# Kernel optimization log

Hardware: AMD Instinct MI355X
Metric: run time of the kernel (lower is better)

## Reference

```python
import jax, jax.numpy as jnp
import numpy as np

N_CLASSES = 3

def setup_inputs() -> dict:
    key = jax.random.key(0)
    k1, k2 = jax.random.split(key)
    feats = jax.random.normal(k1, (16, 1024, 1024, 3), dtype=jnp.float32)
    inst = jax.random.randint(k2, (16, 1024, 1024, 1), 0, N_CLASSES, dtype=jnp.int32)
    return {"feats": feats, "inst": inst}

def reference(feats, inst):
    # Faithful to the TF layer: for each class c, compute the GLOBAL mean of
    # feats over all masked elements (mask tiled across the 3 channels, over
    # the whole batch), then scatter that scalar back into masked positions.
    # Class masks are disjoint, so the sequential update order is benign.
    for c in range(N_CLASSES):
        mask = (inst == c)                                   # [B,H,W,1]
        maskb = jnp.broadcast_to(mask, feats.shape)          # [B,H,W,3]
        cnt = jnp.sum(maskb.astype(feats.dtype))             # scalar count (incl. channels)
        feats_mean = jnp.sum(jnp.where(maskb, feats, 0)) / cnt
        feats = jnp.where(maskb, feats_mean, feats)
    return feats
```

## Files before the change

### kernel.cpp

```cpp
#include <hip/hip_runtime.h>


#define RBLK 2048

typedef float vfloat4 __attribute__((ext_vector_type(4)));
typedef int vint4 __attribute__((ext_vector_type(4)));

__device__ inline double wred_d(double v) {
#pragma unroll
    for (int off = 32; off; off >>= 1) v += __shfl_down(v, off, 64);
    return v;
}
__device__ inline unsigned wred_u(unsigned v) {
#pragma unroll
    for (int off = 32; off; off >>= 1) v += __shfl_down(v, off, 64);
    return v;
}

__global__ __launch_bounds__(256) void reduce_k(const float* __restrict__ feats,
                                                const int* __restrict__ inst,
                                                double* __restrict__ psum,
                                                unsigned* __restrict__ pcnt,
                                                unsigned char* __restrict__ codes,
                                                int npix4) {
    int tid = blockIdx.x * 256 + threadIdx.x;
    int stride = gridDim.x * 256;
    double s0 = 0.0, s1 = 0.0, s2 = 0.0;
    unsigned c0 = 0, c1 = 0, c2 = 0;
    const vint4* inst4 = (const vint4*)inst;
    for (int i = tid; i < npix4; i += stride) {
        vint4 cls = inst4[i];
        const vfloat4* f = (const vfloat4*)(feats + (size_t)i * 12);
        vfloat4 a = f[0], b = f[1], c = f[2];
        double d0 = (double)(a.x + a.y + a.z);
        double d1 = (double)(a.w + b.x + b.y);
        double d2 = (double)(b.z + b.w + c.x);
        double d3 = (double)(c.y + c.z + c.w);
        s0 += (cls.x == 0) ? d0 : 0.0;
        s1 += (cls.x == 1) ? d0 : 0.0;
        s2 += (cls.x == 2) ? d0 : 0.0;
        s0 += (cls.y == 0) ? d1 : 0.0;
        s1 += (cls.y == 1) ? d1 : 0.0;
        s2 += (cls.y == 2) ? d1 : 0.0;
        s0 += (cls.z == 0) ? d2 : 0.0;
        s1 += (cls.z == 1) ? d2 : 0.0;
        s2 += (cls.z == 2) ? d2 : 0.0;
        s0 += (cls.w == 0) ? d3 : 0.0;
        s1 += (cls.w == 1) ? d3 : 0.0;
        s2 += (cls.w == 2) ? d3 : 0.0;
        c0 += (unsigned)(cls.x == 0) + (unsigned)(cls.y == 0) +
              (unsigned)(cls.z == 0) + (unsigned)(cls.w == 0);
        c1 += (unsigned)(cls.x == 1) + (unsigned)(cls.y == 1) +
              (unsigned)(cls.z == 1) + (unsigned)(cls.w == 1);
        c2 += (unsigned)(cls.x == 2) + (unsigned)(cls.y == 2) +
              (unsigned)(cls.z == 2) + (unsigned)(cls.w == 2);
        codes[i] = (unsigned char)((cls.x & 3) | ((cls.y & 3) << 2) |
                                   ((cls.z & 3) << 4) | ((cls.w & 3) << 6));
    }
    s0 = wred_d(s0); s1 = wred_d(s1); s2 = wred_d(s2);
    c0 = wred_u(c0); c1 = wred_u(c1); c2 = wred_u(c2);

    __shared__ double ls[4][3];
    __shared__ unsigned lc[4][3];
    int wid = threadIdx.x >> 6;
    int lane = threadIdx.x & 63;
    if (lane == 0) {
        ls[wid][0] = s0; ls[wid][1] = s1; ls[wid][2] = s2;
        lc[wid][0] = c0; lc[wid][1] = c1; lc[wid][2] = c2;
    }
    __syncthreads();
    if (threadIdx.x < 3) {
        int c = threadIdx.x;
        double s = ls[0][c] + ls[1][c] + ls[2][c] + ls[3][c];
        unsigned cc = lc[0][c] + lc[1][c] + lc[2][c] + lc[3][c];
        psum[blockIdx.x * 3 + c] = s;
        pcnt[blockIdx.x * 3 + c] = cc;
    }
}

__global__ __launch_bounds__(256) void finalize_k(const double* __restrict__ psum,
                                                  const unsigned* __restrict__ pcnt,
                                                  float* __restrict__ mean,
                                                  int nblk) {
    double s0 = 0.0, s1 = 0.0, s2 = 0.0;
    unsigned c0 = 0, c1 = 0, c2 = 0;
    for (int i = threadIdx.x; i < nblk; i += 256) {
        s0 += psum[i * 3 + 0]; s1 += psum[i * 3 + 1]; s2 += psum[i * 3 + 2];
        c0 += pcnt[i * 3 + 0]; c1 += pcnt[i * 3 + 1]; c2 += pcnt[i * 3 + 2];
    }
    s0 = wred_d(s0); s1 = wred_d(s1); s2 = wred_d(s2);
    c0 = wred_u(c0); c1 = wred_u(c1); c2 = wred_u(c2);

    __shared__ double ls[4][3];
    __shared__ unsigned lc[4][3];
    int wid = threadIdx.x >> 6;
    int lane = threadIdx.x & 63;
    if (lane == 0) {
        ls[wid][0] = s0; ls[wid][1] = s1; ls[wid][2] = s2;
        lc[wid][0] = c0; lc[wid][1] = c1; lc[wid][2] = c2;
    }
    __syncthreads();
    if (threadIdx.x < 3) {
        int c = threadIdx.x;
        double s = ls[0][c] + ls[1][c] + ls[2][c] + ls[3][c];
        unsigned cc = lc[0][c] + lc[1][c] + lc[2][c] + lc[3][c];
        mean[c] = (float)(s / (3.0 * (double)cc));
    }
}

__global__ __launch_bounds__(256) void scatter_k(const unsigned short* __restrict__ codes2,
                                                 const float* __restrict__ mean,
                                                 float* __restrict__ out,
                                                 int npix8) {
    int i = blockIdx.x * 256 + threadIdx.x;
    if (i >= npix8) return;
    float m0 = mean[0], m1 = mean[1], m2 = mean[2];
    unsigned cc = codes2[i];
    float v[8];
#pragma unroll
    for (int p = 0; p < 8; ++p) {
        unsigned k = (cc >> (2 * p)) & 3;
        v[p] = (k == 1) ? m1 : ((k == 2) ? m2 : m0);
    }
    vfloat4* o = (vfloat4*)(out + (size_t)i * 24);
    vfloat4 o0 = {v[0], v[0], v[0], v[1]};
    vfloat4 o1 = {v[1], v[1], v[2], v[2]};
    vfloat4 o2 = {v[2], v[3], v[3], v[3]};
    vfloat4 o3 = {v[4], v[4], v[4], v[5]};
    vfloat4 o4 = {v[5], v[5], v[6], v[6]};
    vfloat4 o5 = {v[6], v[7], v[7], v[7]};
    o[0] = o0; o[1] = o1; o[2] = o2; o[3] = o3; o[4] = o4; o[5] = o5;
}

extern "C" void kernel_launch(void* const* d_in, const int* in_sizes, int n_in,
                              void* d_out, int out_size, void* d_ws, size_t ws_size,
                              hipStream_t stream) {
    const float* feats = (const float*)d_in[0];
    const int* inst = (const int*)d_in[1];
    float* out = (float*)d_out;

    int npix = in_sizes[1];
    int npix4 = npix >> 2;
    int npix8 = npix >> 3;

    double* psum = (double*)d_ws;
    unsigned* pcnt = (unsigned*)(psum + RBLK * 3);
    float* mean = (float*)(pcnt + RBLK * 3);
    unsigned char* codes = (unsigned char*)(mean + 4);

    reduce_k<<<RBLK, 256, 0, stream>>>(feats, inst, psum, pcnt, codes, npix4);
    finalize_k<<<1, 256, 0, stream>>>(psum, pcnt, mean, RBLK);
    scatter_k<<<(npix8 + 255) / 256, 256, 0, stream>>>((const unsigned short*)codes, mean,
                                                       out, npix8);
}
```

Baseline: 415.9 us.

## Fuse finalize into scatter and process 8 pixels per reduce iteration

Removes the single-block finalize kernel: every scatter block now redundantly reduces the 2048 per-block partials to compute the class means in shared memory, then writes the output in a grid-stride loop over a fixed grid. The reduce kernel now handles 8 pixels per iteration and writes 16-bit codes directly. This saves one kernel launch and the serial single-block gap, at the cost of each scatter block re-reading the partial sums (about 72KB per block, mostly served from cache).

```diff
diff --git a/kernel.cpp b/kernel.cpp
--- a/kernel.cpp
+++ b/kernel.cpp
@@ -17,45 +17,58 @@
     return v;
 }
 
+__device__ inline void acc_group(vint4 cls, vfloat4 a, vfloat4 b, vfloat4 c,
+                                 double& s0, double& s1, double& s2,
+                                 unsigned& c0, unsigned& c1, unsigned& c2) {
+    double d0 = (double)(a.x + a.y + a.z);
+    double d1 = (double)(a.w + b.x + b.y);
+    double d2 = (double)(b.z + b.w + c.x);
+    double d3 = (double)(c.y + c.z + c.w);
+    s0 += (cls.x == 0) ? d0 : 0.0;
+    s1 += (cls.x == 1) ? d0 : 0.0;
+    s2 += (cls.x == 2) ? d0 : 0.0;
+    s0 += (cls.y == 0) ? d1 : 0.0;
+    s1 += (cls.y == 1) ? d1 : 0.0;
+    s2 += (cls.y == 2) ? d1 : 0.0;
+    s0 += (cls.z == 0) ? d2 : 0.0;
+    s1 += (cls.z == 1) ? d2 : 0.0;
+    s2 += (cls.z == 2) ? d2 : 0.0;
+    s0 += (cls.w == 0) ? d3 : 0.0;
+    s1 += (cls.w == 1) ? d3 : 0.0;
+    s2 += (cls.w == 2) ? d3 : 0.0;
+    c0 += (unsigned)(cls.x == 0) + (unsigned)(cls.y == 0) +
+          (unsigned)(cls.z == 0) + (unsigned)(cls.w == 0);
+    c1 += (unsigned)(cls.x == 1) + (unsigned)(cls.y == 1) +
+          (unsigned)(cls.z == 1) + (unsigned)(cls.w == 1);
+    c2 += (unsigned)(cls.x == 2) + (unsigned)(cls.y == 2) +
+          (unsigned)(cls.z == 2) + (unsigned)(cls.w == 2);
+}
+
+__device__ inline unsigned pack4(vint4 cls) {
+    return (unsigned)((cls.x & 3) | ((cls.y & 3) << 2) |
+                      ((cls.z & 3) << 4) | ((cls.w & 3) << 6));
+}
+
 __global__ __launch_bounds__(256) void reduce_k(const float* __restrict__ feats,
                                                 const int* __restrict__ inst,
                                                 double* __restrict__ psum,
                                                 unsigned* __restrict__ pcnt,
-                                                unsigned char* __restrict__ codes,
-                                                int npix4) {
+                                                unsigned short* __restrict__ codes2,
+                                                int npix8) {
     int tid = blockIdx.x * 256 + threadIdx.x;
     int stride = gridDim.x * 256;
     double s0 = 0.0, s1 = 0.0, s2 = 0.0;
     unsigned c0 = 0, c1 = 0, c2 = 0;
     const vint4* inst4 = (const vint4*)inst;
-    for (int i = tid; i < npix4; i += stride) {
-        vint4 cls = inst4[i];
-        const vfloat4* f = (const vfloat4*)(feats + (size_t)i * 12);
-        vfloat4 a = f[0], b = f[1], c = f[2];
-        double d0 = (double)(a.x + a.y + a.z);
-        double d1 = (double)(a.w + b.x + b.y);
-        double d2 = (double)(b.z + b.w + c.x);
-        double d3 = (double)(c.y + c.z + c.w);
-        s0 += (cls.x == 0) ? d0 : 0.0;
-        s1 += (cls.x == 1) ? d0 : 0.0;
-        s2 += (cls.x == 2) ? d0 : 0.0;
-        s0 += (cls.y == 0) ? d1 : 0.0;
-        s1 += (cls.y == 1) ? d1 : 0.0;
-        s2 += (cls.y == 2) ? d1 : 0.0;
-        s0 += (cls.z == 0) ? d2 : 0.0;
-        s1 += (cls.z == 1) ? d2 : 0.0;
-        s2 += (cls.z == 2) ? d2 : 0.0;
-        s0 += (cls.w == 0) ? d3 : 0.0;
-        s1 += (cls.w == 1) ? d3 : 0.0;
-        s2 += (cls.w == 2) ? d3 : 0.0;
-        c0 += (unsigned)(cls.x == 0) + (unsigned)(cls.y == 0) +
-              (unsigned)(cls.z == 0) + (unsigned)(cls.w == 0);
-        c1 += (unsigned)(cls.x == 1) + (unsigned)(cls.y == 1) +
-              (unsigned)(cls.z == 1) + (unsigned)(cls.w == 1);
-        c2 += (unsigned)(cls.x == 2) + (unsigned)(cls.y == 2) +
-              (unsigned)(cls.z == 2) + (unsigned)(cls.w == 2);
-        codes[i] = (unsigned char)((cls.x & 3) | ((cls.y & 3) << 2) |
-                                   ((cls.z & 3) << 4) | ((cls.w & 3) << 6));
+    for (int i = tid; i < npix8; i += stride) {
+        vint4 clsA = inst4[(size_t)i * 2 + 0];
+        vint4 clsB = inst4[(size_t)i * 2 + 1];
+        const vfloat4* f = (const vfloat4*)(feats + (size_t)i * 24);
+        vfloat4 fa0 = f[0], fa1 = f[1], fa2 = f[2];
+        vfloat4 fb0 = f[3], fb1 = f[4], fb2 = f[5];
+        acc_group(clsA, fa0, fa1, fa2, s0, s1, s2, c0, c1, c2);
+        acc_group(clsB, fb0, fb1, fb2, s0, s1, s2, c0, c1, c2);
+        codes2[i] = (unsigned short)(pack4(clsA) | (pack4(clsB) << 8));
     }
     s0 = wred_d(s0); s1 = wred_d(s1); s2 = wred_d(s2);
     c0 = wred_u(c0); c1 = wred_u(c1); c2 = wred_u(c2);
@@ -78,10 +91,11 @@
     }
 }
 
-__global__ __launch_bounds__(256) void finalize_k(const double* __restrict__ psum,
-                                                  const unsigned* __restrict__ pcnt,
-                                                  float* __restrict__ mean,
-                                                  int nblk) {
+__global__ __launch_bounds__(256) void scatter_k(const double* __restrict__ psum,
+                                                 const unsigned* __restrict__ pcnt,
+                                                 const unsigned short* __restrict__ codes2,
+                                                 float* __restrict__ out,
+                                                 int nblk, int npix8) {
     double s0 = 0.0, s1 = 0.0, s2 = 0.0;
     unsigned c0 = 0, c1 = 0, c2 = 0;
     for (int i = threadIdx.x; i < nblk; i += 256) {
@@ -93,6 +107,7 @@
 
     __shared__ double ls[4][3];
     __shared__ unsigned lc[4][3];
+    __shared__ float lmean[3];
     int wid = threadIdx.x >> 6;
     int lane = threadIdx.x & 63;
     if (lane == 0) {
@@ -104,32 +119,30 @@
         int c = threadIdx.x;
         double s = ls[0][c] + ls[1][c] + ls[2][c] + ls[3][c];
         unsigned cc = lc[0][c] + lc[1][c] + lc[2][c] + lc[3][c];
-        mean[c] = (float)(s / (3.0 * (double)cc));
+        lmean[c] = (float)(s / (3.0 * (double)cc));
     }
-}
+    __syncthreads();
+    float m0 = lmean[0], m1 = lmean[1], m2 = lmean[2];
 
-__global__ __launch_bounds__(256) void scatter_k(const unsigned short* __restrict__ codes2,
-                                                 const float* __restrict__ mean,
-                                                 float* __restrict__ out,
-                                                 int npix8) {
-    int i = blockIdx.x * 256 + threadIdx.x;
-    if (i >= npix8) return;
-    float m0 = mean[0], m1 = mean[1], m2 = mean[2];
-    unsigned cc = codes2[i];
-    float v[8];
+    int tid = blockIdx.x * 256 + threadIdx.x;
+    int stride = gridDim.x * 256;
+    for (int i = tid; i < npix8; i += stride) {
+        unsigned cc8 = codes2[i];
+        float v[8];
 #pragma unroll
-    for (int p = 0; p < 8; ++p) {
-        unsigned k = (cc >> (2 * p)) & 3;
-        v[p] = (k == 1) ? m1 : ((k == 2) ? m2 : m0);
+        for (int p = 0; p < 8; ++p) {
+            unsigned k = (cc8 >> (2 * p)) & 3;
+            v[p] = (k == 1) ? m1 : ((k == 2) ? m2 : m0);
+        }
+        vfloat4* o = (vfloat4*)(out + (size_t)i * 24);
+        vfloat4 o0 = {v[0], v[0], v[0], v[1]};
+        vfloat4 o1 = {v[1], v[1], v[2], v[2]};
+        vfloat4 o2 = {v[2], v[3], v[3], v[3]};
+        vfloat4 o3 = {v[4], v[4], v[4], v[5]};
+        vfloat4 o4 = {v[5], v[5], v[6], v[6]};
+        vfloat4 o5 = {v[6], v[7], v[7], v[7]};
+        o[0] = o0; o[1] = o1; o[2] = o2; o[3] = o3; o[4] = o4; o[5] = o5;
     }
-    vfloat4* o = (vfloat4*)(out + (size_t)i * 24);
-    vfloat4 o0 = {v[0], v[0], v[0], v[1]};
-    vfloat4 o1 = {v[1], v[1], v[2], v[2]};
-    vfloat4 o2 = {v[2], v[3], v[3], v[3]};
-    vfloat4 o3 = {v[4], v[4], v[4], v[5]};
-    vfloat4 o4 = {v[5], v[5], v[6], v[6]};
-    vfloat4 o5 = {v[6], v[7], v[7], v[7]};
-    o[0] = o0; o[1] = o1; o[2] = o2; o[3] = o3; o[4] = o4; o[5] = o5;
 }
 
 extern "C" void kernel_launch(void* const* d_in, const int* in_sizes, int n_in,
@@ -140,16 +153,12 @@
     float* out = (float*)d_out;
 
     int npix = in_sizes[1];
-    int npix4 = npix >> 2;
     int npix8 = npix >> 3;
 
     double* psum = (double*)d_ws;
     unsigned* pcnt = (unsigned*)(psum + RBLK * 3);
-    float* mean = (float*)(pcnt + RBLK * 3);
-    unsigned char* codes = (unsigned char*)(mean + 4);
+    unsigned short* codes2 = (unsigned short*)(pcnt + RBLK * 3);
 
-    reduce_k<<<RBLK, 256, 0, stream>>>(feats, inst, psum, pcnt, codes, npix4);
-    finalize_k<<<1, 256, 0, stream>>>(psum, pcnt, mean, RBLK);
-    scatter_k<<<(npix8 + 255) / 256, 256, 0, stream>>>((const unsigned short*)codes, mean,
-                                                       out, npix8);
+    reduce_k<<<RBLK, 256, 0, stream>>>(feats, inst, psum, pcnt, codes2, npix8);
+    scatter_k<<<RBLK, 256, 0, stream>>>(psum, pcnt, codes2, out, RBLK, npix8);
 }
```

Result: no change. 414.2 us (-0.4%).
